# Kernel tuning notes

Hardware: AMD Instinct MI355X
Metric: run time of the kernel (lower is better)

The kernel has to match this reference:

```python
import jax, jax.numpy as jnp
import numpy as np

BATCH, SEQ_LEN, VEC_DIM, WIDTH = 64, 256, 512, 3


def setup_inputs() -> dict:
    key = jax.random.key(0)
    k = jax.random.split(key, 8)
    F0r = jax.random.normal(k[0], (BATCH, SEQ_LEN, VEC_DIM), jnp.float32)
    F1r = jax.random.normal(k[1], (BATCH, SEQ_LEN, VEC_DIM), jnp.float32)
    sent0_mask = (jax.random.uniform(k[2], (BATCH, SEQ_LEN)) < 0.9).astype(jnp.float32)
    sent1_mask = (jax.random.uniform(k[3], (BATCH, SEQ_LEN)) < 0.9).astype(jnp.float32)
    # nn.Parameter(torch.randn(seq_len, vec_dim))
    W0 = jax.random.normal(k[4], (SEQ_LEN, VEC_DIM), jnp.float32)
    W1 = jax.random.normal(k[5], (SEQ_LEN, VEC_DIM), jnp.float32)
    # Conv2d(2, 1, kernel_size=(WIDTH, 1)) default init: U(-1/sqrt(fan_in), +)
    bound = 1.0 / np.sqrt(2 * WIDTH * 1)
    conv_w = jax.random.uniform(k[6], (1, 2, WIDTH, 1), jnp.float32, -bound, bound)
    conv_b = jax.random.uniform(k[7], (1,), jnp.float32, -bound, bound)
    return dict(F0r=F0r, F1r=F1r, sent0_mask=sent0_mask, sent1_mask=sent1_mask,
                W0=W0, W1=W1, conv_w=conv_w, conv_b=conv_b)


def _conv_tanh_pool(x, conv_w, conv_b):
    # x: [B, 2, S, D]; conv pad (WIDTH-1, 0) -> [B, 1, S+WIDTH-1, D]
    y = jax.lax.conv_general_dilated(
        x, conv_w, window_strides=(1, 1),
        padding=((WIDTH - 1, WIDTH - 1), (0, 0)),
        dimension_numbers=('NCHW', 'OIHW', 'NCHW'))
    y = jnp.tanh(y + conv_b[None, :, None, None])
    # AvgPool2d kernel (WIDTH,1), stride 1 -> [B, 1, S, D]
    y = jax.lax.reduce_window(y, 0.0, jax.lax.add,
                              (1, 1, WIDTH, 1), (1, 1, 1, 1), 'VALID') / WIDTH
    return y[:, 0]  # squeeze channel -> [B, S, D]


def reference(F0r, F1r, sent0_mask, sent1_mask, W0, W1, conv_w, conv_b):
    # masking is in-place in the torch code, so masked F0/F1 feed the conv too
    F0 = F0r * sent0_mask[:, :, None]  # [B, S, D]
    F1 = F1r * sent1_mask[:, :, None]
    # pairwise L2 via ||u-v||^2 = ||u||^2 + ||v||^2 - 2 u.v (avoids [B,S,S,D])
    sq0 = jnp.sum(F0 * F0, axis=-1)  # [B, S]
    sq1 = jnp.sum(F1 * F1, axis=-1)
    cross = jnp.einsum('bid,bjd->bij', F0, F1)  # [B, S, S]
    d2 = jnp.maximum(sq0[:, :, None] + sq1[:, None, :] - 2.0 * cross, 0.0)
    norm = jnp.where(d2 > 0, jnp.sqrt(jnp.where(d2 > 0, d2, 1.0)), 0.0)
    A = 1.0 / (1.0 + norm)  # [B, S, S]
    F0a = jnp.einsum('bij,id->bjd', A, W0)  # A^T @ W0
    F1a = jnp.einsum('bij,jd->bid', A, W1)  # A @ W1
    x0 = jnp.stack([F0, F0a], axis=1)  # [B, 2, S, D]
    x1 = jnp.stack([F1, F1a], axis=1)
    out0 = _conv_tanh_pool(x0, conv_w, conv_b)
    out1 = _conv_tanh_pool(x1, conv_w, conv_b)
    return out0, out1
```

## Files before the change

kernel.cpp:

```cpp
#include <hip/hip_runtime.h>

typedef unsigned short u16;
typedef __attribute__((ext_vector_type(8))) short short8;
typedef __attribute__((ext_vector_type(4))) float f32x4;

__device__ inline u16 f2bf(float f) {
    union { float f; unsigned u; } v; v.f = f;
    unsigned u = v.u;
    unsigned r = (u + 0x7FFFu + ((u >> 16) & 1u)) >> 16;
    return (u16)r;
}
__device__ inline float bf2f(u16 h) {
    union { unsigned u; float f; } v; v.u = ((unsigned)h) << 16;
    return v.f;
}
__device__ inline float frcp(float x) { return __builtin_amdgcn_rcpf(x); }
__device__ inline float fsqrt(float x) { return __builtin_amdgcn_sqrtf(x); }
__device__ inline float ftanh(float x) {
    float e = __expf(2.f * x);
    return 1.f - 2.f * frcp(e + 1.f);
}
__device__ inline float4 bf4f(ushort4 u) {
    float4 f; f.x = bf2f(u.x); f.y = bf2f(u.y); f.z = bf2f(u.z); f.w = bf2f(u.w);
    return f;
}

typedef const __attribute__((address_space(1))) void* gas_ptr;
typedef __attribute__((address_space(3))) void* las_ptr;
__device__ __forceinline__ void gl2lds16(const u16* g, u16* l) {
    __builtin_amdgcn_global_load_lds((gas_ptr)(const void*)g, (las_ptr)(void*)l, 16, 0, 0);
}

__global__ __launch_bounds__(128) void prep_kernel(
    const float* __restrict__ F0r, const float* __restrict__ F1r,
    const float* __restrict__ m0, const float* __restrict__ m1,
    const float* __restrict__ W0, const float* __restrict__ W1,
    u16* __restrict__ F0b, u16* __restrict__ F1b,
    u16* __restrict__ WT0, u16* __restrict__ WT1,
    float* __restrict__ sq0, float* __restrict__ sq1)
{
    int bx = blockIdx.x;
    int t = threadIdx.x;
    if (bx >= 16384) {
        __shared__ u16 Wl[64][40];
        int idx2 = bx - 16384;
        int a = idx2 >> 6;
        int tile = idx2 & 63;
        int s0 = (tile >> 3) * 32, d0 = (tile & 7) * 64;
        const float* W = a ? W1 : W0;
        u16* WT = a ? WT1 : WT0;
        #pragma unroll
        for (int i = 0; i < 4; ++i) {
            int idx = i * 512 + t * 4;
            int sl = idx >> 6, dl = idx & 63;
            float4 v = *(const float4*)(W + (size_t)(s0 + sl) * 512 + d0 + dl);
            Wl[dl + 0][sl] = f2bf(v.x);
            Wl[dl + 1][sl] = f2bf(v.y);
            Wl[dl + 2][sl] = f2bf(v.z);
            Wl[dl + 3][sl] = f2bf(v.w);
        }
        __syncthreads();
        #pragma unroll
        for (int i = 0; i < 4; ++i) {
            int idx = i * 512 + t * 4;
            int dl = idx >> 5, sl = idx & 31;
            ushort4 v;
            v.x = Wl[dl][sl + 0]; v.y = Wl[dl][sl + 1];
            v.z = Wl[dl][sl + 2]; v.w = Wl[dl][sl + 3];
            *(ushort4*)(WT + (size_t)(d0 + dl) * 256 + s0 + sl) = v;
        }
        return;
    }
    int bs = bx;
    size_t base = (size_t)bs * 512 + t * 4;
    float mk0 = m0[bs], mk1 = m1[bs];
    float4 v0 = *(const float4*)(F0r + base);
    float4 v1 = *(const float4*)(F1r + base);
    v0.x *= mk0; v0.y *= mk0; v0.z *= mk0; v0.w *= mk0;
    v1.x *= mk1; v1.y *= mk1; v1.z *= mk1; v1.w *= mk1;
    ushort4 u0; u0.x = f2bf(v0.x); u0.y = f2bf(v0.y); u0.z = f2bf(v0.z); u0.w = f2bf(v0.w);
    ushort4 u1; u1.x = f2bf(v1.x); u1.y = f2bf(v1.y); u1.z = f2bf(v1.z); u1.w = f2bf(v1.w);
    *(ushort4*)(F0b + base) = u0;
    *(ushort4*)(F1b + base) = u1;
    float s0p = v0.x*v0.x + v0.y*v0.y + v0.z*v0.z + v0.w*v0.w;
    float s1p = v1.x*v1.x + v1.y*v1.y + v1.z*v1.z + v1.w*v1.w;
    #pragma unroll
    for (int off = 32; off > 0; off >>= 1) {
        s0p += __shfl_xor(s0p, off);
        s1p += __shfl_xor(s1p, off);
    }
    __shared__ float red0[2], red1[2];
    if ((t & 63) == 0) { red0[t >> 6] = s0p; red1[t >> 6] = s1p; }
    __syncthreads();
    if (t == 0) { sq0[bs] = red0[0] + red0[1]; sq1[bs] = red1[0] + red1[1]; }
}

__global__ __launch_bounds__(256) void gemm_cross_kernel(
    const u16* __restrict__ F0b, const u16* __restrict__ F1b,
    const float* __restrict__ sq0, const float* __restrict__ sq1,
    u16* __restrict__ Abf, u16* __restrict__ ATbf)
{
    __shared__ __align__(16) u16 smem[4 * 8192];

    int b = blockIdx.y;
    int i0 = (blockIdx.x >> 2) * 64, j0 = (blockIdx.x & 3) * 64;
    const u16* Ap = F0b + (size_t)b * 131072;
    const u16* Bp = F1b + (size_t)b * 131072;
    const float* sqR = sq0 + b * 256;
    const float* sqC = sq1 + b * 256;

    const int t = threadIdx.x;
    const int lane = t & 63, w = t >> 6;
    const int wm = w >> 1, wn = w & 1;
    const int q = lane >> 4, lm = lane & 15;

#define STAGE_AB(bufo, k0) do {                                                \
    _Pragma("unroll")                                                          \
    for (int i_ = 0; i_ < 4; ++i_) {                                           \
        int idx_ = i_ * 256 + t;                                               \
        int row_ = idx_ >> 4, seg_ = idx_ & 15;                                \
        int ss_  = seg_ ^ (row_ & 7);                                          \
        int lo_  = (bufo) + (i_ * 256 + w * 64) * 8;         \
        gl2lds16(Ap + (size_t)(i0 + row_) * 512 + (k0) + ss_ * 8,              \
                 &smem[lo_]);                                                  \
        gl2lds16(Bp + (size_t)(j0 + row_) * 512 + (k0) + ss_ * 8,              \
                 &smem[lo_ + 8192]);                                           \
    } } while (0)

    f32x4 acc[2][2];
    #pragma unroll
    for (int x = 0; x < 2; ++x)
        #pragma unroll
        for (int y = 0; y < 2; ++y)
            acc[x][y] = (f32x4){0.f, 0.f, 0.f, 0.f};

    STAGE_AB(0, 0);

    #pragma unroll
    for (int c = 0; c < 4; ++c) {
        __syncthreads();
        if (c < 3)
            STAGE_AB(((c + 1) & 1) * 16384, (c + 1) * 128);
        const int cb = (c & 1) * 16384;
        #pragma unroll
        for (int ks = 0; ks < 128; ks += 32) {
            short8 af[2], bfr[2];
            #pragma unroll
            for (int x = 0; x < 2; ++x) {
                int ra = wm * 32 + x * 16 + lm;
                int rb = wn * 32 + x * 16 + lm;
                int su = (((ks >> 3) + q) ^ (lm & 7)) * 8;
                af[x]  = *(const short8*)&smem[cb + ra * 128 + su];
                bfr[x] = *(const short8*)&smem[cb + 8192 + rb * 128 + su];
            }
            #pragma unroll
            for (int x = 0; x < 2; ++x)
                #pragma unroll
                for (int y = 0; y < 2; ++y)
                    acc[x][y] = __builtin_amdgcn_mfma_f32_16x16x32_bf16(
                        af[x], bfr[y], acc[x][y], 0, 0, 0);
        }
    }
    __syncthreads();
#undef STAGE_AB

    u16 (*Ct)[136] = (u16(*)[136])smem;
    #pragma unroll
    for (int x = 0; x < 2; ++x) {
        #pragma unroll
        for (int r = 0; r < 4; ++r) {
            int ir = wm * 32 + x * 16 + q * 4 + r;
            float si = sqR[i0 + ir];
            #pragma unroll
            for (int y = 0; y < 2; ++y) {
                int jc = wn * 32 + y * 16 + lm;
                float d2 = si + sqC[j0 + jc] - 2.f * acc[x][y][r];
                d2 = fmaxf(d2, 0.f);
                float a = frcp(1.f + fsqrt(d2));
                Ct[ir][jc] = f2bf(a);
            }
        }
    }
    __syncthreads();

    u16* Aout  = Abf  + (size_t)b * 65536;
    u16* ATout = ATbf + (size_t)b * 65536;
    int ii = t >> 2;
    int c0 = (t & 3) * 16;
    #pragma unroll
    for (int c = 0; c < 4; ++c) {
        ushort4 v = *(ushort4*)&Ct[ii][c0 + c * 4];
        *(ushort4*)&Aout[(size_t)(i0 + ii) * 256 + j0 + c0 + c * 4] = v;
    }
    #pragma unroll
    for (int c = 0; c < 4; ++c) {
        ushort4 v;
        v.x = Ct[c0 + c * 4 + 0][ii];
        v.y = Ct[c0 + c * 4 + 1][ii];
        v.z = Ct[c0 + c * 4 + 2][ii];
        v.w = Ct[c0 + c * 4 + 3][ii];
        *(ushort4*)&ATout[(size_t)(j0 + ii) * 256 + i0 + c0 + c * 4] = v;
    }
}

__global__ __launch_bounds__(256) void fa_conv_kernel(
    const u16* __restrict__ Abf, const u16* __restrict__ ATbf,
    const u16* __restrict__ WT0, const u16* __restrict__ WT1,
    const u16* __restrict__ F0b, const u16* __restrict__ F1b,
    const float* __restrict__ cw, const float* __restrict__ cb,
    float* __restrict__ out)
{
    __shared__ __align__(16) u16 Al[36][264];
    __shared__ __align__(16) u16 BlBuf[2 * 8192];
    __shared__ __align__(16) u16 Fl[36][132];

    int b = blockIdx.y, side = blockIdx.z;
    int s0 = blockIdx.x * 32;
    const u16* Ap = (side ? Abf : ATbf) + (size_t)b * 65536;
    const u16* WT = side ? WT1 : WT0;
    const u16* Fb = (side ? F1b : F0b) + (size_t)b * 131072;
    float* o = out + (size_t)side * 8388608 + (size_t)b * 131072;

    const int t = threadIdx.x;
    const int lane = t & 63, w = t >> 6;
    const int q = lane >> 4, lm = lane & 15;

#define STAGE_B(bufo, nn, kb) do {                                             \
    _Pragma("unroll")                                                          \
    for (int i_ = 0; i_ < 4; ++i_) {                                           \
        int idx_ = i_ * 256 + t;                                               \
        int r_ = idx_ >> 3, seg_ = idx_ & 7;                                   \
        int ss_ = seg_ ^ (r_ & 7);                                             \
        gl2lds16(WT + (size_t)((nn) + r_) * 256 + (kb) + ss_ * 8,              \
                 &BlBuf[(bufo) + (i_ * 256 + w * 64) * 8]);                    \
    } } while (0)

    #pragma unroll
    for (int i = 0; i < 5; ++i) {
        int idx = i * 256 + t;
        if (idx < 1152) {
            int r = idx >> 5;
            int seg = idx & 31;
            int s = s0 - 2 + r;
            uint4 v = {0u, 0u, 0u, 0u};
            if ((unsigned)s < 256u)
                v = *(const uint4*)(Ap + (size_t)s * 256 + seg * 8);
            *(uint4*)&Al[r][seg * 8] = v;
        }
    }

    const u16* aRow[3];
    aRow[0] = &Al[lm][0];
    aRow[1] = &Al[16 + lm][0];
    aRow[2] = &Al[(lm < 4) ? (32 + lm) : 0][0];

    float w00 = cw[0], w01 = cw[1], w02 = cw[2];
    float w10 = cw[3], w11 = cw[4], w12 = cw[5];
    float bias = cb[0];
    const float third = 1.f / 3.f;
    const int g = t >> 5;
    const int dl = (t & 31) * 4;

    STAGE_B(0, 0, 0);

    for (int n0 = 0; n0 < 512; n0 += 128) {
        f32x4 acc[3][2];
        #pragma unroll
        for (int x = 0; x < 3; ++x)
            #pragma unroll
            for (int y = 0; y < 2; ++y)
                acc[x][y] = (f32x4){0.f, 0.f, 0.f, 0.f};

        #pragma unroll
        for (int kb_i = 0; kb_i < 4; ++kb_i) {
            __syncthreads();
            if (kb_i < 3)
                STAGE_B(((kb_i + 1) & 1) * 8192, n0, (kb_i + 1) * 64);
            const int cbuf = (kb_i & 1) * 8192;
            const int kb = kb_i * 64;
            #pragma unroll
            for (int ks = 0; ks < 64; ks += 32) {
                short8 af[3], bfr[2];
                #pragma unroll
                for (int x = 0; x < 3; ++x)
                    af[x] = *(const short8*)(aRow[x] + kb + ks + q * 8);
                #pragma unroll
                for (int y = 0; y < 2; ++y) {
                    int rb = w * 32 + y * 16 + lm;
                    int su = (((ks >> 3) + q) ^ (lm & 7)) * 8;
                    bfr[y] = *(const short8*)&BlBuf[cbuf + rb * 64 + su];
                }
                #pragma unroll
                for (int x = 0; x < 3; ++x)
                    #pragma unroll
                    for (int y = 0; y < 2; ++y)
                        acc[x][y] = __builtin_amdgcn_mfma_f32_16x16x32_bf16(
                            af[x], bfr[y], acc[x][y], 0, 0, 0);
            }
        }

        ushort4 frg[8];
        #pragma unroll
        for (int k = 0; k < 8; ++k) {
            int s = s0 + g * 4 - 2 + k;
            ushort4 z = {0, 0, 0, 0};
            frg[k] = ((unsigned)s < 256u)
                   ? *(const ushort4*)(Fb + (size_t)s * 512 + n0 + dl) : z;
        }

        #pragma unroll
        for (int x = 0; x < 3; ++x)
            #pragma unroll
            for (int r = 0; r < 4; ++r) {
                int m = x * 16 + q * 4 + r;
                if (m < 36) {
                    #pragma unroll
                    for (int y = 0; y < 2; ++y)
                        Fl[m][w * 32 + y * 16 + lm] = f2bf(acc[x][y][r]);
                }
            }
        __syncthreads();

        if (n0 < 384)
            STAGE_B(0, n0 + 128, 0);

        float4 f[8], a[8];
        #pragma unroll
        for (int k = 0; k < 8; ++k) {
            f[k] = bf4f(frg[k]);
            a[k] = bf4f(*(const ushort4*)&Fl[g * 4 + k][dl]);
        }
        float4 ty[6];
        #pragma unroll
        for (int k = 0; k < 6; ++k) {
            float4 y;
            y.x = bias + w00*f[k].x + w01*f[k+1].x + w02*f[k+2].x + w10*a[k].x + w11*a[k+1].x + w12*a[k+2].x;
            y.y = bias + w00*f[k].y + w01*f[k+1].y + w02*f[k+2].y + w10*a[k].y + w11*a[k+1].y + w12*a[k+2].y;
            y.z = bias + w00*f[k].z + w01*f[k+1].z + w02*f[k+2].z + w10*a[k].z + w11*a[k+1].z + w12*a[k+2].z;
            y.w = bias + w00*f[k].w + w01*f[k+1].w + w02*f[k+2].w + w10*a[k].w + w11*a[k+1].w + w12*a[k+2].w;
            y.x = ftanh(y.x); y.y = ftanh(y.y); y.z = ftanh(y.z); y.w = ftanh(y.w);
            ty[k] = y;
        }
        #pragma unroll
        for (int r = 0; r < 4; ++r) {
            float4 res;
            res.x = (ty[r].x + ty[r+1].x + ty[r+2].x) * third;
            res.y = (ty[r].y + ty[r+1].y + ty[r+2].y) * third;
            res.z = (ty[r].z + ty[r+1].z + ty[r+2].z) * third;
            res.w = (ty[r].w + ty[r+1].w + ty[r+2].w) * third;
            *(float4*)(o + (size_t)(s0 + g * 4 + r) * 512 + n0 + dl) = res;
        }
    }
#undef STAGE_B
}

extern "C" void kernel_launch(void* const* d_in, const int* in_sizes, int n_in,
                              void* d_out, int out_size, void* d_ws, size_t ws_size,
                              hipStream_t stream)
{
    const float* F0r = (const float*)d_in[0];
    const float* F1r = (const float*)d_in[1];
    const float* m0  = (const float*)d_in[2];
    const float* m1  = (const float*)d_in[3];
    const float* W0  = (const float*)d_in[4];
    const float* W1  = (const float*)d_in[5];
    const float* cw  = (const float*)d_in[6];
    const float* cb  = (const float*)d_in[7];
    float* out = (float*)d_out;

    char* ws = (char*)d_ws;
    u16* F0b   = (u16*)(ws);
    u16* F1b   = (u16*)(ws + 16777216);
    u16* Abf   = (u16*)(ws + 33554432);
    u16* ATbf  = (u16*)(ws + 41943040);
    float* sq0 = (float*)(ws + 50331648);
    float* sq1 = (float*)(ws + 50397184);
    u16* WT0   = (u16*)(ws + 50462720);
    u16* WT1   = (u16*)(ws + 50724864);

    prep_kernel<<<16512, 128, 0, stream>>>(F0r, F1r, m0, m1, W0, W1,
                                           F0b, F1b, WT0, WT1, sq0, sq1);
    gemm_cross_kernel<<<dim3(16, 64), 256, 0, stream>>>(F0b, F1b, sq0, sq1, Abf, ATbf);
    fa_conv_kernel<<<dim3(8, 64, 2), 256, 0, stream>>>(Abf, ATbf, WT0, WT1,
                                                       F0b, F1b, cw, cb, out);
}
```

Baseline: 184.3 us.

## Fuse cross-distance GEMM into the attention-conv kernel, recomputing A tiles per block

Removes the separate gemm_cross kernel and the A/AT bf16 round-trip through global memory. Each fa_conv block now computes its own 36-row halo strip of the distance matrix against all 256 columns of the other sentence, applies the 1/(1+sqrt) transform, and writes it directly into shared memory. This trades global writes and reads of A plus one launch for redundant recomputation of the halo rows and a single-buffered, non-overlapped K loop that loads the full 256x64 slab per step. Both sides now compute the same cross products independently, so total GEMM work roughly doubles.

```diff
diff --git a/kernel.cpp b/kernel.cpp
--- a/kernel.cpp
+++ b/kernel.cpp
@@ -95,128 +95,24 @@
     if (t == 0) { sq0[bs] = red0[0] + red0[1]; sq1[bs] = red1[0] + red1[1]; }
 }
 
-__global__ __launch_bounds__(256) void gemm_cross_kernel(
+__global__ __launch_bounds__(256) void fused_kernel(
     const u16* __restrict__ F0b, const u16* __restrict__ F1b,
     const float* __restrict__ sq0, const float* __restrict__ sq1,
-    u16* __restrict__ Abf, u16* __restrict__ ATbf)
-{
-    __shared__ __align__(16) u16 smem[4 * 8192];
-
-    int b = blockIdx.y;
-    int i0 = (blockIdx.x >> 2) * 64, j0 = (blockIdx.x & 3) * 64;
-    const u16* Ap = F0b + (size_t)b * 131072;
-    const u16* Bp = F1b + (size_t)b * 131072;
-    const float* sqR = sq0 + b * 256;
-    const float* sqC = sq1 + b * 256;
-
-    const int t = threadIdx.x;
-    const int lane = t & 63, w = t >> 6;
-    const int wm = w >> 1, wn = w & 1;
-    const int q = lane >> 4, lm = lane & 15;
-
-#define STAGE_AB(bufo, k0) do {                                                \
-    _Pragma("unroll")                                                          \
-    for (int i_ = 0; i_ < 4; ++i_) {                                           \
-        int idx_ = i_ * 256 + t;                                               \
-        int row_ = idx_ >> 4, seg_ = idx_ & 15;                                \
-        int ss_  = seg_ ^ (row_ & 7);                                          \
-        int lo_  = (bufo) + (i_ * 256 + w * 64) * 8;         \
-        gl2lds16(Ap + (size_t)(i0 + row_) * 512 + (k0) + ss_ * 8,              \
-                 &smem[lo_]);                                                  \
-        gl2lds16(Bp + (size_t)(j0 + row_) * 512 + (k0) + ss_ * 8,              \
-                 &smem[lo_ + 8192]);                                           \
-    } } while (0)
-
-    f32x4 acc[2][2];
-    #pragma unroll
-    for (int x = 0; x < 2; ++x)
-        #pragma unroll
-        for (int y = 0; y < 2; ++y)
-            acc[x][y] = (f32x4){0.f, 0.f, 0.f, 0.f};
-
-    STAGE_AB(0, 0);
-
-    #pragma unroll
-    for (int c = 0; c < 4; ++c) {
-        __syncthreads();
-        if (c < 3)
-            STAGE_AB(((c + 1) & 1) * 16384, (c + 1) * 128);
-        const int cb = (c & 1) * 16384;
-        #pragma unroll
-        for (int ks = 0; ks < 128; ks += 32) {
-            short8 af[2], bfr[2];
-            #pragma unroll
-            for (int x = 0; x < 2; ++x) {
-                int ra = wm * 32 + x * 16 + lm;
-                int rb = wn * 32 + x * 16 + lm;
-                int su = (((ks >> 3) + q) ^ (lm & 7)) * 8;
-                af[x]  = *(const short8*)&smem[cb + ra * 128 + su];
-                bfr[x] = *(const short8*)&smem[cb + 8192 + rb * 128 + su];
-            }
-            #pragma unroll
-            for (int x = 0; x < 2; ++x)
-                #pragma unroll
-                for (int y = 0; y < 2; ++y)
-                    acc[x][y] = __builtin_amdgcn_mfma_f32_16x16x32_bf16(
-                        af[x], bfr[y], acc[x][y], 0, 0, 0);
-        }
-    }
-    __syncthreads();
-#undef STAGE_AB
-
-    u16 (*Ct)[136] = (u16(*)[136])smem;
-    #pragma unroll
-    for (int x = 0; x < 2; ++x) {
-        #pragma unroll
-        for (int r = 0; r < 4; ++r) {
-            int ir = wm * 32 + x * 16 + q * 4 + r;
-            float si = sqR[i0 + ir];
-            #pragma unroll
-            for (int y = 0; y < 2; ++y) {
-                int jc = wn * 32 + y * 16 + lm;
-                float d2 = si + sqC[j0 + jc] - 2.f * acc[x][y][r];
-                d2 = fmaxf(d2, 0.f);
-                float a = frcp(1.f + fsqrt(d2));
-                Ct[ir][jc] = f2bf(a);
-            }
-        }
-    }
-    __syncthreads();
-
-    u16* Aout  = Abf  + (size_t)b * 65536;
-    u16* ATout = ATbf + (size_t)b * 65536;
-    int ii = t >> 2;
-    int c0 = (t & 3) * 16;
-    #pragma unroll
-    for (int c = 0; c < 4; ++c) {
-        ushort4 v = *(ushort4*)&Ct[ii][c0 + c * 4];
-        *(ushort4*)&Aout[(size_t)(i0 + ii) * 256 + j0 + c0 + c * 4] = v;
-    }
-    #pragma unroll
-    for (int c = 0; c < 4; ++c) {
-        ushort4 v;
-        v.x = Ct[c0 + c * 4 + 0][ii];
-        v.y = Ct[c0 + c * 4 + 1][ii];
-        v.z = Ct[c0 + c * 4 + 2][ii];
-        v.w = Ct[c0 + c * 4 + 3][ii];
-        *(ushort4*)&ATout[(size_t)(j0 + ii) * 256 + i0 + c0 + c * 4] = v;
-    }
-}
-
-__global__ __launch_bounds__(256) void fa_conv_kernel(
-    const u16* __restrict__ Abf, const u16* __restrict__ ATbf,
     const u16* __restrict__ WT0, const u16* __restrict__ WT1,
-    const u16* __restrict__ F0b, const u16* __restrict__ F1b,
+    const u16* __restrict__ F0b2, const u16* __restrict__ F1b2,
     const float* __restrict__ cw, const float* __restrict__ cb,
     float* __restrict__ out)
 {
     __shared__ __align__(16) u16 Al[36][264];
-    __shared__ __align__(16) u16 BlBuf[2 * 8192];
-    __shared__ __align__(16) u16 Fl[36][132];
+    __shared__ __align__(16) u16 region[21136];
+    u16 (*Fl)[132] = (u16(*)[132])(region + 16384);
 
     int b = blockIdx.y, side = blockIdx.z;
     int s0 = blockIdx.x * 32;
-    const u16* Ap = (side ? Abf : ATbf) + (size_t)b * 65536;
+    const u16* Sp  = (side ? F0b : F1b) + (size_t)b * 131072;
+    const u16* Gp  = (side ? F1b : F0b) + (size_t)b * 131072;
+    const float* sqS = (side ? sq0 : sq1) + b * 256;
+    const float* sqG = (side ? sq1 : sq0) + b * 256;
     const u16* WT = side ? WT1 : WT0;
     const u16* Fb = (side ? F1b : F0b) + (size_t)b * 131072;
     float* o = out + (size_t)side * 8388608 + (size_t)b * 131072;
@@ -224,6 +120,82 @@
     const int t = threadIdx.x;
     const int lane = t & 63, w = t >> 6;
     const int q = lane >> 4, lm = lane & 15;
+
+    f32x4 acc1[3][4];
+    #pragma unroll
+    for (int x = 0; x < 3; ++x)
+        #pragma unroll
+        for (int cn = 0; cn < 4; ++cn)
+            acc1[x][cn] = (f32x4){0.f, 0.f, 0.f, 0.f};
+
+    for (int kc = 0; kc < 512; kc += 64) {
+        __syncthreads();
+        #pragma unroll
+        for (int i = 0; i < 8; ++i) {
+            int idx = i * 256 + t;
+            int r = idx >> 3, seg = idx & 7;
+            int ss = seg ^ (r & 7);
+            gl2lds16(Gp + (size_t)r * 512 + kc + ss * 8,
+                     &region[(i * 256 + w * 64) * 8]);
+        }
+        {
+            int idx = t;
+            int r = idx >> 3, seg = idx & 7;
+            int ss = seg ^ (r & 7);
+            int s = s0 - 2 + r; s = s < 0 ? 0 : (s > 255 ? 255 : s);
+            gl2lds16(Sp + (size_t)s * 512 + kc + ss * 8,
+                     &region[16384 + (w * 64) * 8]);
+        }
+        if (t < 128) {
+            int idx = 256 + t;
+            int r = idx >> 3, seg = idx & 7;
+            int ss = seg ^ (r & 7);
+            int s = s0 - 2 + r; s = s < 0 ? 0 : (s > 255 ? 255 : s);
+            gl2lds16(Sp + (size_t)s * 512 + kc + ss * 8,
+                     &region[16384 + (256 + w * 64) * 8]);
+        }
+        __syncthreads();
+        #pragma unroll
+        for (int ks = 0; ks < 64; ks += 32) {
+            int su = (((ks >> 3) + q) ^ (lm & 7)) * 8;
+            short8 af[3], bfr[4];
+            #pragma unroll
+            for (int x = 0; x < 3; ++x)
+                af[x] = *(const short8*)&region[16384 + (x * 16 + lm) * 64 + su];
+            #pragma unroll
+            for (int cn = 0; cn < 4; ++cn)
+                bfr[cn] = *(const short8*)&region[(w * 64 + cn * 16 + lm) * 64 + su];
+            #pragma unroll
+            for (int x = 0; x < 3; ++x)
+                #pragma unroll
+                for (int cn = 0; cn < 4; ++cn)
+                    acc1[x][cn] = __builtin_amdgcn_mfma_f32_16x16x32_bf16(
+                        af[x], bfr[cn], acc1[x][cn], 0, 0, 0);
+        }
+    }
+    __syncthreads();
+
+    float sqg[4];
+    #pragma unroll
+    for (int cn = 0; cn < 4; ++cn) sqg[cn] = sqG[w * 64 + cn * 16 + lm];
+    #pragma unroll
+    for (int x = 0; x < 3; ++x) {
+        #pragma unroll
+        for (int r = 0; r < 4; ++r) {
+            int m = x * 16 + q * 4 + r;
+            if (m < 36) {
+                int s = s0 - 2 + m;
+                bool ok = (unsigned)s < 256u;
+                float sqs = ok ? sqS[s] : 0.f;
+                #pragma unroll
+                for (int cn = 0; cn < 4; ++cn) {
+                    float d2 = fmaxf(sqs + sqg[cn] - 2.f * acc1[x][cn][r], 0.f);
+                    float a = ok ? frcp(1.f + fsqrt(d2)) : 0.f;
+                    Al[m][w * 64 + cn * 16 + lm] = f2bf(a);
+                }
+            }
+        }
+    }
 
 #define STAGE_B(bufo, nn, kb) do {                                             \
     _Pragma("unroll")                                                          \
@@ -232,22 +204,8 @@
         int r_ = idx_ >> 3, seg_ = idx_ & 7;                                   \
         int ss_ = seg_ ^ (r_ & 7);                                             \
         gl2lds16(WT + (size_t)((nn) + r_) * 256 + (kb) + ss_ * 8,              \
-                 &BlBuf[(bufo) + (i_ * 256 + w * 64) * 8]);                    \
+                 &region[(bufo) + (i_ * 256 + w * 64) * 8]);                   \
     } } while (0)
-
-    #pragma unroll
-    for (int i = 0; i < 5; ++i) {
-        int idx = i * 256 + t;
-        if (idx < 1152) {
-            int r = idx >> 5;
-            int seg = idx & 31;
-            int s = s0 - 2 + r;
-            uint4 v = {0u, 0u, 0u, 0u};
-            if ((unsigned)s < 256u)
-                v = *(const uint4*)(Ap + (size_t)s * 256 + seg * 8);
-            *(uint4*)&Al[r][seg * 8] = v;
-        }
-    }
 
     const u16* aRow[3];
     aRow[0] = &Al[lm][0];
@@ -288,7 +246,7 @@
                 for (int y = 0; y < 2; ++y) {
                     int rb = w * 32 + y * 16 + lm;
                     int su = (((ks >> 3) + q) ^ (lm & 7)) * 8;
-                    bfr[y] = *(const short8*)&BlBuf[cbuf + rb * 64 + su];
+                    bfr[y] = *(const short8*)&region[cbuf + rb * 64 + su];
                 }
                 #pragma unroll
                 for (int x = 0; x < 3; ++x)
@@ -371,8 +329,6 @@
     char* ws = (char*)d_ws;
     u16* F0b   = (u16*)(ws);
     u16* F1b   = (u16*)(ws + 16777216);
-    u16* Abf   = (u16*)(ws + 33554432);
-    u16* ATbf  = (u16*)(ws + 41943040);
     float* sq0 = (float*)(ws + 50331648);
     float* sq1 = (float*)(ws + 50397184);
     u16* WT0   = (u16*)(ws + 50462720);
@@ -380,7 +336,7 @@
 
     prep_kernel<<<16512, 128, 0, stream>>>(F0r, F1r, m0, m1, W0, W1,
                                            F0b, F1b, WT0, WT1, sq0, sq1);
-    gemm_cross_kernel<<<dim3(16, 64), 256, 0, stream>>>(F0b, F1b, sq0, sq1, Abf, ATbf);
-    fa_conv_kernel<<<dim3(8, 64, 2), 256, 0, stream>>>(Abf, ATbf, WT0, WT1,
-                                                       F0b, F1b, cw, cb, out);
-}
+    fused_kernel<<<dim3(8, 64, 2), 256, 0, stream>>>(F0b, F1b, sq0, sq1,
+                                                     WT0, WT1, F0b, F1b,
+                                                     cw, cb, out);
+}
```

Measured after the change: 208.1 us. +12.9%, slower.
